# Performance work log

Measured on AMD Instinct MI355X. Metric: run time of the kernel, lower is better.

## Reference

```python
import jax, jax.numpy as jnp
from jax import lax
import numpy as np

DN = ('NCHW', 'OIHW', 'NCHW')
LEAKY_SLOPE = 0.01  # torch nn.LeakyReLU default


def conv(x, w, b=None, stride=1, pad=0):
    y = lax.conv_general_dilated(x, w, (stride, stride), [(pad, pad), (pad, pad)],
                                 dimension_numbers=DN)
    return y if b is None else y + b[None, :, None, None]


def conv_transpose2d(x, w, b):
    # torch ConvTranspose2d(k=4, s=2, p=1); w layout (Cin, Cout, 4, 4)
    wf = jnp.transpose(jnp.flip(w, (2, 3)), (1, 0, 2, 3))  # -> OIHW
    y = lax.conv_general_dilated(x, wf, (1, 1), [(2, 2), (2, 2)],
                                 lhs_dilation=(2, 2), dimension_numbers=DN)
    return y + b[None, :, None, None]


def residual_stack(x, rw3, rw1):
    # 6 ResidualLayers: x + conv1x1(relu(conv3x3(x))), both convs bias-free
    for i in range(rw3.shape[0]):
        h = jax.nn.relu(conv(x, rw3[i], pad=1))
        x = x + conv(h, rw1[i])
    return x


def vector_quantize(latents, codebook):
    # latents: [B, D, H, W] -> NHWC
    lat = jnp.transpose(latents, (0, 2, 3, 1))
    B, H, W, D = lat.shape
    flat = lat.reshape(-1, D)  # [N, D]
    # pairwise squared distances [N, K]
    dist = (jnp.sum(flat ** 2, axis=1, keepdims=True)
            + jnp.sum(codebook ** 2, axis=1)
            - 2.0 * flat @ codebook.T)
    inds = jnp.argmin(dist, axis=1)            # [N]
    q = codebook[inds].reshape(B, H, W, D)     # gather == one-hot matmul
    commitment_loss = jnp.mean((lax.stop_gradient(q) - lat) ** 2)
    embedding_loss = jnp.mean((q - lax.stop_gradient(lat)) ** 2)
    q_st = lat + lax.stop_gradient(q - lat)    # straight-through
    return jnp.transpose(q_st, (0, 3, 1, 2)), embedding_loss, commitment_loss


def setup_inputs() -> dict:
    key = jax.random.key(0)
    ks = iter(jax.random.split(key, 32))
    B, C, S = 16, 3, 128
    H0, H1 = 128, 256          # hidden_dims
    D, K = 64, 512             # embedding_dim, num_embeddings
    n_res = 6

    def w(shape, scale=0.05):
        return (jax.random.normal(next(ks), shape, dtype=jnp.float32) * scale)

    inp = {
        'x': jax.random.normal(next(ks), (B, C, S, S), dtype=jnp.float32),
        # encoder
        'ew0': w((H0, C, 4, 4)), 'eb0': jnp.zeros((H0,), jnp.float32),
        'ew1': w((H1, H0, 4, 4)), 'eb1': jnp.zeros((H1,), jnp.float32),
        'ew2': w((H1, H1, 3, 3)), 'eb2': jnp.zeros((H1,), jnp.float32),
        'erw3': w((n_res, H1, H1, 3, 3)),
        'erw1': w((n_res, H1, H1, 1, 1)),
        'ew3': w((D, H1, 1, 1)), 'eb3': jnp.zeros((D,), jnp.float32),
        # codebook, uniform(-1/K, 1/K) as in torch init
        'codebook': jax.random.uniform(next(ks), (K, D), jnp.float32, -1.0 / K, 1.0 / K),
        # decoder
        'dw0': w((H1, D, 3, 3)), 'db0': jnp.zeros((H1,), jnp.float32),
        'drw3': w((n_res, H1, H1, 3, 3)),
        'drw1': w((n_res, H1, H1, 1, 1)),
        'tw0': w((H1, H0, 4, 4)), 'tb0': jnp.zeros((H0,), jnp.float32),
        'tw1': w((H0, C, 4, 4)), 'tb1': jnp.zeros((C,), jnp.float32),
    }
    return inp


def reference(x, ew0, eb0, ew1, eb1, ew2, eb2, erw3, erw1, ew3, eb3,
              codebook, dw0, db0, drw3, drw1, tw0, tb0, tw1, tb1):
    lrelu = lambda t: jax.nn.leaky_relu(t, LEAKY_SLOPE)
    # encoder: two stride-2 downsamples, conv3x3, 6 residuals, 1x1 -> D
    h = lrelu(conv(x, ew0, eb0, stride=2, pad=1))   # [B,128,64,64]
    h = lrelu(conv(h, ew1, eb1, stride=2, pad=1))   # [B,256,32,32]
    h = lrelu(conv(h, ew2, eb2, stride=1, pad=1))
    h = residual_stack(h, erw3, erw1)
    h = lrelu(h)
    z = lrelu(conv(h, ew3, eb3))                    # [B,64,32,32]
    # vector quantization
    q, embedding_loss, commitment_loss = vector_quantize(z, codebook)
    # decoder
    d = lrelu(conv(q, dw0, db0, stride=1, pad=1))   # [B,256,32,32]
    d = residual_stack(d, drw3, drw1)
    d = lrelu(d)
    d = lrelu(conv_transpose2d(d, tw0, tb0))        # [B,128,64,64]
    recons = jnp.tanh(conv_transpose2d(d, tw1, tb1))  # [B,3,128,128]
    return recons, embedding_loss, commitment_loss
```

## Files before the change

### kernel.cpp

```cpp
#include <hip/hip_runtime.h>
#include <math.h>


typedef __attribute__((ext_vector_type(8))) short bf16x8;
typedef __attribute__((ext_vector_type(4))) float f32x4;

__device__ __forceinline__ float bf2f(short s) {
    unsigned u = ((unsigned)(unsigned short)s) << 16;
    return __builtin_bit_cast(float, u);
}
__device__ __forceinline__ unsigned short f2bfu(float f) {
    unsigned u = __builtin_bit_cast(unsigned, f);
    u = (u + 0x7fff + ((u >> 16) & 1)) >> 16;
    return (unsigned short)u;
}
__device__ __forceinline__ short f2bf(float f) { return (short)f2bfu(f); }
__device__ __forceinline__ int pack2(float a, float b) {
    return (int)f2bfu(a) | ((int)f2bfu(b) << 16);
}

template<int ACT>
__device__ __forceinline__ float actf(float v) {
    if (ACT == 1) return fmaxf(v, 0.f);
    if (ACT == 2) return v > 0.f ? v : 0.01f * v;
    return v;
}

__device__ __forceinline__ void gload_lds16(const void* g, void* l) {
    __builtin_amdgcn_global_load_lds(
        (const __attribute__((address_space(1))) unsigned int*)g,
        (__attribute__((address_space(3))) unsigned int*)l, 16, 0, 0);
}

__device__ __forceinline__ int fof(int r) { return (r & 3) ^ ((r >> 2) & 3); }

#define WAITV(N) asm volatile("s_waitcnt vmcnt(" #N ")" ::: "memory")
#define LGKM0 asm volatile("s_waitcnt lgkmcnt(0)" ::: "memory")

__device__ __forceinline__ void prep_t(const float* __restrict__ src,
        short* __restrict__ dst, int COUT, int CIN, int T, int TP,
        int blk, float* sT, int tid) {
    int opc = COUT >> 2;
    int c = blk / opc, oc0 = (blk - c * opc) * 4;
    const float* s = src + ((size_t)c * COUT + oc0) * CIN * T;
    int n = 4 * CIN * T;
    for (int i = tid; i < n; i += 256) {
        int ocl = i / (CIN * T); int rem = i - ocl * (CIN * T);
        int ic = rem / T, t = rem - ic * T;
        sT[(ocl * CIN + ic) * TP + t] = s[i];
    }
    __syncthreads();
    for (int i = tid; i < n; i += 256) {
        int t = i / (4 * CIN); int rem = i - t * (4 * CIN);
        int ocl = rem / CIN, ic = rem - ocl * CIN;
        dst[(((size_t)c * T + t) * COUT + oc0 + ocl) * CIN + ic]
            = f2bf(sT[(ocl * CIN + ic) * TP + t]);
    }
    __syncthreads();
}

__global__ __launch_bounds__(256) void prep_all_k(
        const float* ew1, const float* ew2, const float* erw3,
        const float* erw1, const float* ew3, const float* dw0,
        const float* drw3, const float* drw1, const float* tw0,
        short* Wp1, short* We2, short* Wer3, short* We11, short* Wz,
        short* Wd0, short* Wdr3, short* Wdr1, short* Wt0) {
    __shared__ float sT[9216];
    int bid = blockIdx.x, tid = threadIdx.x;
    if (bid < 64)        prep_t(ew1, Wp1, 256, 128, 16, 17, bid, sT, tid);
    else if (bid < 128)  prep_t(ew2, We2, 256, 256, 9, 9, bid - 64, sT, tid);
    else if (bid < 512)  prep_t(erw3, Wer3, 256, 256, 9, 9, bid - 128, sT, tid);
    else if (bid < 896)  prep_t(erw1, We11, 256, 256, 1, 1, bid - 512, sT, tid);
    else if (bid < 912)  prep_t(ew3, Wz, 64, 256, 1, 1, bid - 896, sT, tid);
    else if (bid < 976)  prep_t(dw0, Wd0, 256, 64, 9, 9, bid - 912, sT, tid);
    else if (bid < 1360) prep_t(drw3, Wdr3, 256, 256, 9, 9, bid - 976, sT, tid);
    else if (bid < 1744) prep_t(drw1, Wdr1, 256, 256, 1, 1, bid - 1360, sT, tid);
    else {
        int i = (bid - 1744) * 256 + tid;
        if (i < 524288) {
            int ic = i & 255; int r = i >> 8;
            int oc = r & 127; r >>= 7;
            int tap = r & 3; int par = r >> 2;
            int py = par >> 1, px = par & 1, my = tap >> 1, mx = tap & 1;
            int ky = 2 * my + (py ^ 1), kx = 2 * mx + (px ^ 1);
            Wt0[i] = f2bf(tw0[(((size_t)ic * 128 + oc) * 4 + ky) * 4 + kx]);
        }
    }
}

__global__ __launch_bounds__(256) void halo_all_k(short* P0, short* PB,
        short* PC, short* Pq) {
    int g = blockIdx.x * 256 + threadIdx.x;
    short* base; int W, C, idx;
    if (g < 135168)      { base = P0; W = 68; C = 128; idx = g; }
    else if (g < 274432) { base = PB; W = 36; C = 256; idx = g - 135168; }
    else if (g < 413696) { base = PC; W = 36; C = 256; idx = g - 274432; }
    else                 { base = Pq; W = 36; C = 64;  idx = g - 413696; }
    int c8 = C >> 3;
    int per_img = (4 * W + (W - 4) * 4) * c8;
    int img = idx / per_img, r = idx - img * per_img;
    int row, off;
    if (r < 4 * W * c8) {
        int rr = r / (W * c8);
        row = (rr < 2) ? rr : W - 4 + rr;
        off = r - rr * (W * c8);
    } else {
        int r2 = r - 4 * W * c8;
        row = 2 + r2 / (4 * c8);
        int q = r2 - (row - 2) * (4 * c8);
        off = (q < 2 * c8) ? q : (W - 2) * c8 + (q - 2 * c8);
    }
    ((int4*)(base + ((size_t)img * W + row) * W * C))[off] = int4{0, 0, 0, 0};
}

template<int CIN, int NTAPS, int TAPPAT, int SM, int INW, int OUTACT,
         bool HASB, bool FUSE>
__global__ __launch_bounds__(1024, 1) void rconv_k(
        const short* __restrict__ in, const short* __restrict__ Wp,
        const float* __restrict__ bias, const short* __restrict__ W1p,
        short* __restrict__ outp) {
    constexpr int CH64 = (CIN >= 128) ? CIN / 64 : 1;
    constexpr int LG2 = (CH64 == 4) ? 2 : (CH64 == 2) ? 1 : 0;
    constexpr int ST = NTAPS * CH64;
    __shared__ short sLds[81920];
    const int tid = threadIdx.x;
    const int lane = tid & 63, wv = tid >> 6;
    const int wc = wv & 3, mh = (wv >> 2) & 1, kg = wv >> 3;
    const int pix0 = blockIdx.x * 64;
    const int l15 = lane & 15, hi = lane >> 4;
    const int sl = hi ^ fof(l15);
    const bool low = (tid < 512);

    const short* Aptr = in;
    if (low) {
        int arow = tid >> 3, aslot = tid & 7;
        int pixa = pix0 + arow;
        int ba = pixa >> 10, Ya = (pixa >> 5) & 31, Xa = pixa & 31;
        Aptr = in + (size_t)((ba * INW + SM * Ya + 2) * INW + (SM * Xa + 2)) * CIN
             + (aslot >> 2) * 32 + (((aslot & 3) ^ fof(arow)) * 8);
    }
    const short* Bptr[2];
#pragma unroll
    for (int j = 0; j < 2; j++) {
        int gb = tid + 1024 * j;
        int kkb = gb >> 10, oc = (gb >> 2) & 255, slb = gb & 3;
        Bptr[j] = Wp + (size_t)oc * CIN + kkb * 32 + ((slb ^ fof(oc)) * 8);
    }

    auto stage = [&](int s, int bi) {
        int t = s >> LG2;
        int c0 = (s & (CH64 - 1)) * 64;
        int rof, cof;
        if (TAPPAT == 1) { rof = t / 3 - 1; cof = t % 3 - 1; }
        else             { rof = (t >> 2) - 1; cof = (t & 3) - 1; }
        char* L = (char*)sLds + bi * 40960;
        if (low)
            gload_lds16(Aptr + (rof * INW + cof) * CIN + c0, L + tid * 16);
        int woff = t * (256 * CIN) + c0;
        gload_lds16(Bptr[0] + woff, L + 8192 + tid * 16);
        gload_lds16(Bptr[1] + woff, L + 8192 + (tid + 1024) * 16);
    };

    f32x4 acc[2][4];
#pragma unroll
    for (int mi = 0; mi < 2; mi++)
#pragma unroll
        for (int ni = 0; ni < 4; ni++) acc[mi][ni] = f32x4{0.f, 0.f, 0.f, 0.f};

    stage(0, 0);
    stage(1, 1);
    int bi = 0;
    for (int s = 0; s < ST; ++s) {
        if (s < ST - 1) { if (low) { WAITV(3); } else { WAITV(2); } }
        else { WAITV(0); }
        __builtin_amdgcn_s_barrier();
        int nx = bi + 2; if (nx >= 3) nx -= 3;
        if (s + 2 < ST) stage(s + 2, nx);
        const short* LA = sLds + bi * 20480;
        const short* LB = LA + 4096;
        bf16x8 af[2], bfr[4];
#pragma unroll
        for (int mi = 0; mi < 2; mi++)
            af[mi] = *(const bf16x8*)(LA + (mh * 32 + mi * 16 + l15) * 64
                                      + kg * 32 + sl * 8);
#pragma unroll
        for (int ni = 0; ni < 4; ni++)
            bfr[ni] = *(const bf16x8*)(LB + kg * 8192
                                       + (wc * 64 + ni * 16 + l15) * 32 + sl * 8);
        __builtin_amdgcn_s_setprio(1);
#pragma unroll
        for (int mi = 0; mi < 2; mi++)
#pragma unroll
            for (int ni = 0; ni < 4; ni++)
                acc[mi][ni] = __builtin_amdgcn_mfma_f32_16x16x32_bf16(
                    af[mi], bfr[ni], acc[mi][ni], 0, 0, 0);
        __builtin_amdgcn_s_setprio(0);
        bi = (bi == 2) ? 0 : bi + 1;
    }

    float* MB = (float*)sLds;

    __syncthreads();
    if (kg == 1) {
#pragma unroll
        for (int mi = 0; mi < 2; mi++)
#pragma unroll
            for (int ni = 0; ni < 4; ni++)
#pragma unroll
                for (int r = 0; r < 4; r++)
                    MB[(mh * 32 + mi * 16 + hi * 4 + r) * 256
                       + wc * 64 + ni * 16 + l15] = acc[mi][ni][r];
    }
    __syncthreads();

    if (!FUSE) {
        if (kg == 0) {
#pragma unroll
            for (int mi = 0; mi < 2; mi++)
#pragma unroll
                for (int ni = 0; ni < 4; ni++) {
                    int col = wc * 64 + ni * 16 + l15;
                    float b = HASB ? bias[col] : 0.f;
#pragma unroll
                    for (int r = 0; r < 4; r++) {
                        int row = mh * 32 + mi * 16 + hi * 4 + r;
                        MB[row * 256 + col] += acc[mi][ni][r] + b;
                    }
                }
        }
        __syncthreads();
#pragma unroll
        for (int j = 0; j < 2; j++) {
            int idx = j * 1024 + tid;
            int p = idx >> 5, c0 = (idx & 31) * 8;
            int pix = pix0 + p;
            int b = pix >> 10, Y = (pix >> 5) & 31, X = pix & 31;
            size_t base = (((size_t)b * 36 + Y + 2) * 36 + X + 2) * 256 + c0;
            const float4* m4 = (const float4*)(MB + p * 256 + c0);
            float4 lo = m4[0], hv = m4[1];
            int pk[4];
            pk[0] = pack2(actf<OUTACT>(lo.x), actf<OUTACT>(lo.y));
            pk[1] = pack2(actf<OUTACT>(lo.z), actf<OUTACT>(lo.w));
            pk[2] = pack2(actf<OUTACT>(hv.x), actf<OUTACT>(hv.y));
            pk[3] = pack2(actf<OUTACT>(hv.z), actf<OUTACT>(hv.w));
            *(int4*)(outp + base) = *(int4*)pk;
        }
        return;
    }

    const short* W1ptr[2];
#pragma unroll
    for (int j = 0; j < 2; j++) {
        int gb = tid + 1024 * j;
        int kkb = gb >> 10, oc = (gb >> 2) & 255, slb = gb & 3;
        W1ptr[j] = W1p + (size_t)oc * 256 + kkb * 32 + ((slb ^ fof(oc)) * 8);
    }
    auto stage2 = [&](int c) {
        char* L = (char*)sLds + 98304 + (c & 1) * 32768;
        gload_lds16(W1ptr[0] + c * 64, L + tid * 16);
        gload_lds16(W1ptr[1] + c * 64, L + (tid + 1024) * 16);
    };
    stage2(0);
    stage2(1);

    short* H = sLds + 32768;
    if (kg == 0) {
#pragma unroll
        for (int mi = 0; mi < 2; mi++)
#pragma unroll
            for (int ni = 0; ni < 4; ni++) {
                int col = wc * 64 + ni * 16 + l15;
#pragma unroll
                for (int r = 0; r < 4; r++) {
                    int row = mh * 32 + mi * 16 + hi * 4 + r;
                    float v = acc[mi][ni][r] + MB[row * 256 + col];
                    H[((col >> 5) * 64 + row) * 32
                      + (((col >> 3) & 3) ^ fof(row)) * 8 + (col & 7)]
                        = f2bf(fmaxf(v, 0.f));
                }
            }
    }
    LGKM0;
    __builtin_amdgcn_sched_barrier(0);
    __builtin_amdgcn_s_barrier();

    f32x4 acc2[2][4];
#pragma unroll
    for (int mi = 0; mi < 2; mi++)
#pragma unroll
        for (int ni = 0; ni < 4; ni++) acc2[mi][ni] = f32x4{0.f, 0.f, 0.f, 0.f};

    for (int s2 = 0; s2 < 4; ++s2) {
        if (s2 < 3) { WAITV(2); } else { WAITV(0); }
        __builtin_amdgcn_s_barrier();
        int c = s2 * 2 + kg;
        const short* LW = sLds + 49152 + (s2 & 1) * 16384 + kg * 8192;
        bf16x8 af2[2], bf2r[4];
#pragma unroll
        for (int mi = 0; mi < 2; mi++) {
            int row = mh * 32 + mi * 16 + l15;
            af2[mi] = *(const bf16x8*)(H + (c * 64 + row) * 32
                                       + (hi ^ fof(row)) * 8);
        }
#pragma unroll
        for (int ni = 0; ni < 4; ni++)
            bf2r[ni] = *(const bf16x8*)(LW + (wc * 64 + ni * 16 + l15) * 32
                                        + sl * 8);
        LGKM0;
        __builtin_amdgcn_sched_barrier(0);
        __builtin_amdgcn_s_barrier();
        if (s2 < 2) stage2(s2 + 2);
        __builtin_amdgcn_s_setprio(1);
#pragma unroll
        for (int mi = 0; mi < 2; mi++)
#pragma unroll
            for (int ni = 0; ni < 4; ni++)
                acc2[mi][ni] = __builtin_amdgcn_mfma_f32_16x16x32_bf16(
                    af2[mi], bf2r[ni], acc2[mi][ni], 0, 0, 0);
        __builtin_amdgcn_s_setprio(0);
    }

    __syncthreads();
    if (kg == 1) {
#pragma unroll
        for (int mi = 0; mi < 2; mi++)
#pragma unroll
            for (int ni = 0; ni < 4; ni++)
#pragma unroll
                for (int r = 0; r < 4; r++)
                    MB[(mh * 32 + mi * 16 + hi * 4 + r) * 256
                       + wc * 64 + ni * 16 + l15] = acc2[mi][ni][r];
    }
    __syncthreads();
    if (kg == 0) {
#pragma unroll
        for (int mi = 0; mi < 2; mi++)
#pragma unroll
            for (int ni = 0; ni < 4; ni++) {
                int col = wc * 64 + ni * 16 + l15;
#pragma unroll
                for (int r = 0; r < 4; r++) {
                    int row = mh * 32 + mi * 16 + hi * 4 + r;
                    MB[row * 256 + col] += acc2[mi][ni][r];
                }
            }
    }
    __syncthreads();
#pragma unroll
    for (int j = 0; j < 2; j++) {
        int idx = j * 1024 + tid;
        int p = idx >> 5, c0 = (idx & 31) * 8;
        int pix = pix0 + p;
        int b = pix >> 10, Y = (pix >> 5) & 31, X = pix & 31;
        size_t base = (((size_t)b * 36 + Y + 2) * 36 + X + 2) * 256 + c0;
        const float4* m4 = (const float4*)(MB + p * 256 + c0);
        float4 lo = m4[0], hv = m4[1];
        bf16x8 rv = *(const bf16x8*)(in + base);
        int pk[4];
        pk[0] = pack2(actf<OUTACT>(lo.x + bf2f(rv[0])),
                      actf<OUTACT>(lo.y + bf2f(rv[1])));
        pk[1] = pack2(actf<OUTACT>(lo.z + bf2f(rv[2])),
                      actf<OUTACT>(lo.w + bf2f(rv[3])));
        pk[2] = pack2(actf<OUTACT>(hv.x + bf2f(rv[4])),
                      actf<OUTACT>(hv.y + bf2f(rv[5])));
        pk[3] = pack2(actf<OUTACT>(hv.z + bf2f(rv[6])),
                      actf<OUTACT>(hv.w + bf2f(rv[7])));
        *(int4*)(outp + base) = *(int4*)pk;
    }
}

template<int CIN, int COUT, int NTAPS, int TAPPAT, int SM, int INW,
         int OUTACT, bool RES, bool HASB, int OUTMODE, int BN>
__global__ __launch_bounds__(256) void gconv_k(
        const short* __restrict__ in, const short* __restrict__ Wp,
        const float* __restrict__ bias, const short* __restrict__ res,
        void* __restrict__ outp) {
    constexpr int KCH = CIN / 32;
    constexpr int LG = (KCH == 8) ? 3 : (KCH == 4) ? 2 : (KCH == 2) ? 1 : 0;
    constexpr int ST = NTAPS * KCH;
    constexpr int NF = BN / 32;
    constexpr int WN = BN / 2;
    __shared__ short sA[3 * 128 * 32];
    __shared__ short sB[3 * BN * 32];
    const int tid = threadIdx.x;
    const int lane = tid & 63, wv = tid >> 6;
    const int wr = wv >> 1, wc = wv & 1;
    const int pix0 = blockIdx.x * 128;
    const int oc0 = blockIdx.y * BN;
    int py = 0, px = 0;
    if (TAPPAT == 3) {
        int par = blockIdx.z;
        py = par >> 1; px = par & 1;
        Wp += (size_t)par * NTAPS * COUT * CIN;
    }
    const int sp = tid >> 2;
    const int swz = ((tid & 3) ^ fof(sp)) * 8;
    int rbA[2];
#pragma unroll
    for (int rd = 0; rd < 2; rd++) {
        int pix = pix0 + sp + rd * 64;
        int b = pix >> 10, Y = (pix >> 5) & 31, X = pix & 31;
        rbA[rd] = ((b * INW + SM * Y + 2) * INW + (SM * X + 2)) * CIN + swz;
    }
    const int wb0 = (oc0 + sp) * CIN + swz;
    const int wb1 = (oc0 + sp + 64) * CIN + swz;

    f32x4 acc[4][NF];
#pragma unroll
    for (int i = 0; i < 4; i++)
#pragma unroll
        for (int j = 0; j < NF; j++) acc[i][j] = f32x4{0.f, 0.f, 0.f, 0.f};

    const int sslot = ((lane >> 4) ^ fof(lane & 15)) * 8;
    const int abase = (wr * 64 + (lane & 15)) * 32 + sslot;
    const int bbase = (wc * WN + (lane & 15)) * 32 + sslot;

    auto stage = [&](int s, int biq) {
        int t = s >> LG, c = s & (KCH - 1);
        int rof, cof;
        if (TAPPAT == 0) { rof = 0; cof = 0; }
        else if (TAPPAT == 1) { rof = t / 3 - 1; cof = t % 3 - 1; }
        else if (TAPPAT == 2) { rof = t / 4 - 1; cof = t % 4 - 1; }
        else { int my = t >> 1, mx = t & 1;
               rof = (py == 0) ? -my : 1 - my;
               cof = (px == 0) ? -mx : 1 - mx; }
        const int tapoff = (rof * INW + cof) * CIN + c * 32;
        char* a = (char*)sA + biq * 8192;
        char* b = (char*)sB + biq * (BN * 64);
        const short* wt = Wp + (size_t)t * COUT * CIN + c * 32;
        gload_lds16(in + rbA[0] + tapoff, a + tid * 16);
        gload_lds16(in + rbA[1] + tapoff, a + 4096 + tid * 16);
        gload_lds16(wt + wb0, b + tid * 16);
        if (BN == 128) gload_lds16(wt + wb1, b + 4096 + tid * 16);
    };

    stage(0, 0);
    stage(1, 1);
    int cur = 0;
    for (int s = 0; s < ST; ++s) {
        if (s < ST - 1) {
            if (BN == 128) { WAITV(4); } else { WAITV(3); }
        } else {
            WAITV(0);
        }
        __builtin_amdgcn_s_barrier();
        int nxt = cur + 2; if (nxt >= 3) nxt -= 3;
        if (s + 2 < ST) stage(s + 2, nxt);
        const short* a = sA + cur * 4096;
        const short* b = sB + cur * (BN * 32);
        bf16x8 af[4], bfm[NF];
#pragma unroll
        for (int mi = 0; mi < 4; mi++)
            af[mi] = *(const bf16x8*)(a + abase + mi * 512);
#pragma unroll
        for (int ni = 0; ni < NF; ni++)
            bfm[ni] = *(const bf16x8*)(b + bbase + ni * 512);
        __builtin_amdgcn_s_setprio(1);
#pragma unroll
        for (int mi = 0; mi < 4; mi++)
#pragma unroll
            for (int ni = 0; ni < NF; ni++)
                acc[mi][ni] = __builtin_amdgcn_mfma_f32_16x16x32_bf16(
                    af[mi], bfm[ni], acc[mi][ni], 0, 0, 0);
        __builtin_amdgcn_s_setprio(0);
        cur = (cur == 2) ? 0 : cur + 1;
    }
#pragma unroll
    for (int mi = 0; mi < 4; mi++) {
#pragma unroll
        for (int r = 0; r < 4; r++) {
            int pix = pix0 + wr * 64 + mi * 16 + (lane >> 4) * 4 + r;
            int b = pix >> 10, Y = (pix >> 5) & 31, X = pix & 31;
            size_t rowoff = 0;
            if (OUTMODE == 0)
                rowoff = (((size_t)b * 36 + Y + 2) * 36 + X + 2) * COUT;
            else if (OUTMODE == 2)
                rowoff = (((size_t)b * 68 + 2 * Y + py + 2) * 68 + 2 * X + px + 2) * 128;
#pragma unroll
            for (int ni = 0; ni < NF; ni++) {
                int col = oc0 + wc * WN + ni * 16 + (lane & 15);
                float v = acc[mi][ni][r];
                if (HASB) v += bias[col];
                if (OUTMODE == 1) {
                    ((float*)outp)[(size_t)pix * COUT + col] = actf<OUTACT>(v);
                } else {
                    size_t off = rowoff + col;
                    if (RES) v += bf2f(res[off]);
                    ((short*)outp)[off] = f2bf(actf<OUTACT>(v));
                }
            }
        }
    }
}

__global__ __launch_bounds__(256) void conv0_k(const float* __restrict__ x,
        const float* __restrict__ W, const float* __restrict__ bias,
        short* __restrict__ P0) {
    __shared__ float sP[3 * 4 * 132];
    __shared__ short sB[8192];
    __shared__ float sMB[8192];
    int y = blockIdx.x, b = blockIdx.y;
    int tid = threadIdx.x;
    int lane = tid & 63, w = tid >> 6;
    int l15 = lane & 15, hi = lane >> 4;
    int sl = hi ^ fof(l15);
    for (int t = tid; t < 8192; t += 256) {
        int oc = t >> 6, k = t & 63;
        float v = (k < 48) ? W[(size_t)oc * 48 + k] : 0.f;
        int kk = k >> 5, slot = (k >> 3) & 3, j = k & 7;
        sB[oc * 64 + kk * 32 + ((slot ^ fof(oc)) * 8) + j] = f2bf(v);
    }
    for (int t = tid; t < 1560; t += 256) {
        int ic = t / 520; int r = t - ic * 520;
        int ry = r / 130, rx = r - ry * 130;
        int iy = 2 * y - 1 + ry, ix = rx - 1;
        float v = 0.f;
        if ((unsigned)iy < 128u && (unsigned)ix < 128u)
            v = x[((size_t)b * 3 + ic) * 16384 + iy * 128 + ix];
        sP[(ic * 4 + ry) * 132 + rx] = v;
    }
    __syncthreads();
    int ox = w * 16 + l15;
    bf16x8 af[2];
#pragma unroll
    for (int kk = 0; kk < 2; kk++) {
        short tmp[8];
#pragma unroll
        for (int j = 0; j < 8; j++) {
            int k = kk * 32 + hi * 8 + j;
            float v = 0.f;
            if (k < 48) {
                int ic = k >> 4, ky = (k >> 2) & 3, kx = k & 3;
                v = sP[(ic * 4 + ky) * 132 + 2 * ox + kx];
            }
            tmp[j] = f2bf(v);
        }
        af[kk] = *(bf16x8*)tmp;
    }
    f32x4 acc[8];
#pragma unroll
    for (int ni = 0; ni < 8; ni++) acc[ni] = f32x4{0.f, 0.f, 0.f, 0.f};
#pragma unroll
    for (int ni = 0; ni < 8; ni++) {
        int oc = ni * 16 + l15;
        bf16x8 b0 = *(const bf16x8*)(sB + oc * 64 + sl * 8);
        bf16x8 b1 = *(const bf16x8*)(sB + oc * 64 + 32 + sl * 8);
        acc[ni] = __builtin_amdgcn_mfma_f32_16x16x32_bf16(af[0], b0, acc[ni], 0, 0, 0);
        acc[ni] = __builtin_amdgcn_mfma_f32_16x16x32_bf16(af[1], b1, acc[ni], 0, 0, 0);
    }
#pragma unroll
    for (int ni = 0; ni < 8; ni++) {
        int col = ni * 16 + l15;
        float bv = bias[col];
#pragma unroll
        for (int r = 0; r < 4; r++)
            sMB[(w * 16 + hi * 4 + r) * 128 + col] = actf<2>(acc[ni][r] + bv);
    }
    __syncthreads();
#pragma unroll
    for (int it = 0; it < 4; it++) {
        int idx = it * 256 + tid;
        int p = idx >> 4, c0 = (idx & 15) * 8;
        size_t base = (((size_t)b * 68 + y + 2) * 68 + p + 2) * 128 + c0;
        const float4* m4 = (const float4*)(sMB + p * 128 + c0);
        float4 lo = m4[0], hv = m4[1];
        int pk[4];
        pk[0] = pack2(lo.x, lo.y); pk[1] = pack2(lo.z, lo.w);
        pk[2] = pack2(hv.x, hv.y); pk[3] = pack2(hv.z, hv.w);
        *(int4*)(P0 + base) = *(int4*)pk;
    }
}

__global__ __launch_bounds__(256) void vq_argmin_k(const float* __restrict__ zr,
        const float* __restrict__ cb, int* __restrict__ ind) {
    __shared__ short sZ[2][128 * 32];
    __shared__ short sC[2][128 * 32];
    __shared__ float sN[128];
    const int tid = threadIdx.x;
    const int lane = tid & 63, wv = tid >> 6;
    const int pos0 = blockIdx.x * 128;
#pragma unroll
    for (int it = 0; it < 4; ++it) {
        int task = tid + it * 256;
        int row = task >> 3, kq = task & 7;
        const float4* zp = (const float4*)(zr + (size_t)(pos0 + row) * 64 + kq * 8);
        float4 v0 = zp[0], v1 = zp[1];
        int slot = ((kq & 3) ^ fof(row)) * 8;
        short tmp[8] = {f2bf(v0.x), f2bf(v0.y), f2bf(v0.z), f2bf(v0.w),
                        f2bf(v1.x), f2bf(v1.y), f2bf(v1.z), f2bf(v1.w)};
        *(bf16x8*)&sZ[kq >> 2][row * 32 + slot] = *(bf16x8*)tmp;
    }
    const int sslot = ((lane >> 4) ^ fof(lane & 15)) * 8;
    const int l15 = lane & 15;
    float best[2][4]; int bidx[2][4];
#pragma unroll
    for (int mi = 0; mi < 2; mi++)
#pragma unroll
        for (int r = 0; r < 4; r++) { best[mi][r] = INFINITY; bidx[mi][r] = 0; }
    for (int ch = 0; ch < 4; ++ch) {
        __syncthreads();
#pragma unroll
        for (int it = 0; it < 4; ++it) {
            int task = tid + it * 256;
            int row = task >> 3, kq = task & 7;
            const float4* cp = (const float4*)(cb + (size_t)(ch * 128 + row) * 64 + kq * 8);
            float4 v0 = cp[0], v1 = cp[1];
            int slot = ((kq & 3) ^ fof(row)) * 8;
            short tmp[8] = {f2bf(v0.x), f2bf(v0.y), f2bf(v0.z), f2bf(v0.w),
                            f2bf(v1.x), f2bf(v1.y), f2bf(v1.z), f2bf(v1.w)};
            *(bf16x8*)&sC[kq >> 2][row * 32 + slot] = *(bf16x8*)tmp;
        }
        if (tid < 128) {
            const float4* cp = (const float4*)(cb + (size_t)(ch * 128 + tid) * 64);
            float s = 0.f;
#pragma unroll
            for (int q = 0; q < 16; q++) {
                float4 v = cp[q];
                s += v.x * v.x + v.y * v.y + v.z * v.z + v.w * v.w;
            }
            sN[tid] = s;
        }
        __syncthreads();
        f32x4 acc[2][8];
#pragma unroll
        for (int mi = 0; mi < 2; mi++)
#pragma unroll
            for (int ni = 0; ni < 8; ni++) acc[mi][ni] = f32x4{0.f, 0.f, 0.f, 0.f};
#pragma unroll
        for (int kc = 0; kc < 2; ++kc) {
            bf16x8 za[2], ca[8];
#pragma unroll
            for (int mi = 0; mi < 2; mi++)
                za[mi] = *(const bf16x8*)&sZ[kc][(wv * 32 + mi * 16 + l15) * 32 + sslot];
#pragma unroll
            for (int ni = 0; ni < 8; ni++)
                ca[ni] = *(const bf16x8*)&sC[kc][(ni * 16 + l15) * 32 + sslot];
#pragma unroll
            for (int mi = 0; mi < 2; mi++)
#pragma unroll
                for (int ni = 0; ni < 8; ni++)
                    acc[mi][ni] = __builtin_amdgcn_mfma_f32_16x16x32_bf16(
                        za[mi], ca[ni], acc[mi][ni], 0, 0, 0);
        }
#pragma unroll
        for (int mi = 0; mi < 2; mi++)
#pragma unroll
            for (int ni = 0; ni < 8; ni++) {
                float nrm = sN[ni * 16 + l15];
                int idx = ch * 128 + ni * 16 + l15;
#pragma unroll
                for (int r = 0; r < 4; r++) {
                    float sc = nrm - 2.f * acc[mi][ni][r];
                    if (sc < best[mi][r]) { best[mi][r] = sc; bidx[mi][r] = idx; }
                }
            }
    }
#pragma unroll
    for (int m = 1; m < 16; m <<= 1) {
#pragma unroll
        for (int mi = 0; mi < 2; mi++)
#pragma unroll
            for (int r = 0; r < 4; r++) {
                float os = __shfl_xor(best[mi][r], m);
                int   oi = __shfl_xor(bidx[mi][r], m);
                if (os < best[mi][r] || (os == best[mi][r] && oi < bidx[mi][r])) {
                    best[mi][r] = os; bidx[mi][r] = oi;
                }
            }
    }
    if (l15 == 0) {
        int g = lane >> 4;
#pragma unroll
        for (int mi = 0; mi < 2; mi++)
#pragma unroll
            for (int r = 0; r < 4; r++)
                ind[pos0 + wv * 32 + mi * 16 + g * 4 + r] = bidx[mi][r];
    }
}

__global__ __launch_bounds__(256) void vq_gather_k(const float* __restrict__ zr,
        const float* __restrict__ cb, const int* __restrict__ ind,
        short* __restrict__ q, float* __restrict__ part) {
    int pos = blockIdx.x * 256 + threadIdx.x;
    int b = pos >> 10, hw = pos & 1023, y = hw >> 5, xx = hw & 31;
    int idx = ind[pos];
    const float4* cp = (const float4*)(cb + (size_t)idx * 64);
    const float4* zp = (const float4*)(zr + (size_t)pos * 64);
    size_t qb = (((size_t)b * 36 + y + 2) * 36 + xx + 2) * 64;
    float sum = 0.f;
#pragma unroll
    for (int d4 = 0; d4 < 16; d4++) {
        float4 c = cp[d4], z = zp[d4];
        float dx = c.x - z.x, dy = c.y - z.y, dz = c.z - z.z, dw = c.w - z.w;
        sum += dx * dx + dy * dy + dz * dz + dw * dw;
        ((int*)(q + qb))[2 * d4] = pack2(c.x, c.y);
        ((int*)(q + qb))[2 * d4 + 1] = pack2(c.z, c.w);
    }
#pragma unroll
    for (int m = 1; m < 64; m <<= 1) sum += __shfl_xor(sum, m);
    __shared__ float sred[4];
    int lane = threadIdx.x & 63, wvv = threadIdx.x >> 6;
    if (lane == 0) sred[wvv] = sum;
    __syncthreads();
    if (threadIdx.x == 0)
        part[blockIdx.x] = sred[0] + sred[1] + sred[2] + sred[3];
}

__global__ void finalize_k(const float* __restrict__ part, float* __restrict__ out) {
    if (threadIdx.x == 0) {
        float s = 0.f;
        for (int k = 0; k < 64; k++) s += part[k];
        float m = s / 1048576.f;
        out[786432] = m;
        out[786433] = m;
    }
}

__global__ __launch_bounds__(256) void tw1_k(const short* __restrict__ in,
        const float* __restrict__ W, const float* __restrict__ bias,
        float* __restrict__ out) {
    __shared__ float sW[16 * 128 * 4];
    int b = blockIdx.y, y0 = blockIdx.x * 8;
    int tid = threadIdx.x;
    for (int t = tid; t < 2048; t += 256) {
        int k = t >> 7, ic = t & 127;
        float4 v;
        v.x = W[((size_t)ic * 3 + 0) * 16 + k];
        v.y = W[((size_t)ic * 3 + 1) * 16 + k];
        v.z = W[((size_t)ic * 3 + 2) * 16 + k];
        v.w = 0.f;
        *(float4*)&sW[t * 4] = v;
    }
    __syncthreads();
    int r = tid >> 5, g = tid & 31;
    int oy = y0 + r, py = oy & 1, Y = oy >> 1, pxp = g & 1;
    float acc[4][3];
#pragma unroll
    for (int p = 0; p < 4; p++)
#pragma unroll
        for (int o = 0; o < 3; o++) acc[p][o] = 0.f;
#pragma unroll
    for (int my = 0; my < 2; my++) {
        int iy = Y + ((py == 0) ? -my : 1 - my) + 2;
        const short* rowp = in + (((size_t)b * 68 + iy) * 68) * 128;
        int ky = 2 * my + (py ^ 1);
#pragma unroll
        for (int mx = 0; mx < 2; mx++) {
            int kx = 2 * mx + (pxp ^ 1);
            int cof = ((pxp == 0) ? -mx : 1 - mx) + 2;
            const float* wbase = &sW[((ky * 4 + kx) * 128) * 4];
            const short* pptr[4];
#pragma unroll
            for (int p = 0; p < 4; p++) {
                int X = ((g + 32 * p) >> 1) + cof;
                pptr[p] = rowp + (size_t)X * 128;
            }
            for (int icb = 0; icb < 16; icb++) {
                bf16x8 v[4];
#pragma unroll
                for (int p = 0; p < 4; p++)
                    v[p] = *(const bf16x8*)(pptr[p] + icb * 8);
#pragma unroll
                for (int j = 0; j < 8; j++) {
                    float4 w = *(const float4*)&wbase[(icb * 8 + j) * 4];
#pragma unroll
                    for (int p = 0; p < 4; p++) {
                        float xv = bf2f(v[p][j]);
                        acc[p][0] += w.x * xv;
                        acc[p][1] += w.y * xv;
                        acc[p][2] += w.z * xv;
                    }
                }
            }
        }
    }
#pragma unroll
    for (int p = 0; p < 4; p++) {
        int ox = g + 32 * p;
#pragma unroll
        for (int o = 0; o < 3; o++)
            out[(((size_t)b * 3 + o) << 14) + oy * 128 + ox] =
                tanhf(acc[p][o] + bias[o]);
    }
}

extern "C" void kernel_launch(void* const* d_in, const int* in_sizes, int n_in,
                              void* d_out, int out_size, void* d_ws, size_t ws_size,
                              hipStream_t stream) {
    const float* x    = (const float*)d_in[0];
    const float* ew0  = (const float*)d_in[1];
    const float* eb0  = (const float*)d_in[2];
    const float* ew1  = (const float*)d_in[3];
    const float* eb1  = (const float*)d_in[4];
    const float* ew2  = (const float*)d_in[5];
    const float* eb2  = (const float*)d_in[6];
    const float* erw3 = (const float*)d_in[7];
    const float* erw1 = (const float*)d_in[8];
    const float* ew3  = (const float*)d_in[9];
    const float* eb3  = (const float*)d_in[10];
    const float* cbk  = (const float*)d_in[11];
    const float* dw0  = (const float*)d_in[12];
    const float* db0  = (const float*)d_in[13];
    const float* drw3 = (const float*)d_in[14];
    const float* drw1 = (const float*)d_in[15];
    const float* tw0  = (const float*)d_in[16];
    const float* tb0  = (const float*)d_in[17];
    const float* tw1  = (const float*)d_in[18];
    const float* tb1  = (const float*)d_in[19];
    float* out = (float*)d_out;

    short* S = (short*)d_ws;
    short* P0  = S;
    short* PB  = P0 + 9469952;
    short* PC  = PB + 5308416;
    short* Pq  = PC + 5308416;
    short* Wp1 = Pq + 1327104;
    short* We2 = Wp1 + 524288;
    short* Wer3 = We2 + 589824;
    short* We11 = Wer3 + 3538944;
    short* Wz   = We11 + 393216;
    short* Wd0  = Wz + 16384;
    short* Wdr3 = Wd0 + 147456;
    short* Wdr1 = Wdr3 + 3538944;
    short* Wt0  = Wdr1 + 393216;
    float* F   = (float*)(S + 31080448);
    float* Zr  = F;
    float* PART = Zr + 1048576;
    int*   IND = (int*)(PART + 64);

    halo_all_k<<<1752, 256, 0, stream>>>(P0, PB, PC, Pq);
    prep_all_k<<<3792, 256, 0, stream>>>(ew1, ew2, erw3, erw1, ew3, dw0,
        drw3, drw1, tw0, Wp1, We2, Wer3, We11, Wz, Wd0, Wdr3, Wdr1, Wt0);

    conv0_k<<<dim3(64, 16), 256, 0, stream>>>(x, ew0, eb0, P0);
    rconv_k<128, 16, 2, 2, 68, 2, true, false>
        <<<256, 1024, 0, stream>>>(P0, Wp1, eb1, nullptr, PB);
    rconv_k<256, 9, 1, 1, 36, 2, true, false>
        <<<256, 1024, 0, stream>>>(PB, We2, eb2, nullptr, PC);
    for (int i = 0; i < 6; i++) {
        short* inb  = (i & 1) ? PB : PC;
        short* outb = (i & 1) ? PC : PB;
        if (i < 5)
            rconv_k<256, 9, 1, 1, 36, 0, false, true>
                <<<256, 1024, 0, stream>>>(inb, Wer3 + (size_t)i * 589824,
                    nullptr, We11 + (size_t)i * 65536, outb);
        else
            rconv_k<256, 9, 1, 1, 36, 2, false, true>
                <<<256, 1024, 0, stream>>>(inb, Wer3 + (size_t)i * 589824,
                    nullptr, We11 + (size_t)i * 65536, outb);
    }
    gconv_k<256, 64, 1, 0, 1, 36, 2, false, true, 1, 64>
        <<<dim3(128, 1), 256, 0, stream>>>(PC, Wz, eb3, nullptr, Zr);

    vq_argmin_k<<<128, 256, 0, stream>>>(Zr, cbk, IND);
    vq_gather_k<<<64, 256, 0, stream>>>(Zr, cbk, IND, Pq, PART);

    rconv_k<64, 9, 1, 1, 36, 2, true, false>
        <<<256, 1024, 0, stream>>>(Pq, Wd0, db0, nullptr, PC);
    for (int i = 0; i < 6; i++) {
        short* inb  = (i & 1) ? PB : PC;
        short* outb = (i & 1) ? PC : PB;
        if (i < 5)
            rconv_k<256, 9, 1, 1, 36, 0, false, true>
                <<<256, 1024, 0, stream>>>(inb, Wdr3 + (size_t)i * 589824,
                    nullptr, Wdr1 + (size_t)i * 65536, outb);
        else
            rconv_k<256, 9, 1, 1, 36, 2, false, true>
                <<<256, 1024, 0, stream>>>(inb, Wdr3 + (size_t)i * 589824,
                    nullptr, Wdr1 + (size_t)i * 65536, outb);
    }
    gconv_k<256, 128, 4, 3, 1, 36, 2, false, true, 2, 128>
        <<<dim3(128, 1, 4), 256, 0, stream>>>(PC, Wt0, tb0, nullptr, P0);
    tw1_k<<<dim3(16, 16), 256, 0, stream>>>(P0, tw1, tb1, out);

    finalize_k<<<1, 64, 0, stream>>>(PART, out);
}
```

Measured before the change: 591.5 us.

## Drop split-K wave groups in rconv_k, use 512-thread blocks with double buffering

The residual/conv kernel drops the two-way K split across wave groups in 1024-thread blocks. It now uses 512-thread blocks where each wave runs the full K loop, two 64-wide k-steps per stage. This removes the LDS partial-sum reduction and its extra barriers in both the 3x3 and fused 1x1 phases, and halves LDS use. In exchange there are half as many waves per CU on a 256-block grid. The load pipeline also goes from triple to double buffering with a full wait each step, and the tighter launch bound may raise register pressure.

```diff
diff --git a/kernel.cpp b/kernel.cpp
--- a/kernel.cpp
+++ b/kernel.cpp
@@ -115,34 +115,33 @@
 
 template<int CIN, int NTAPS, int TAPPAT, int SM, int INW, int OUTACT,
          bool HASB, bool FUSE>
-__global__ __launch_bounds__(1024, 1) void rconv_k(
+__global__ __launch_bounds__(512, 4) void rconv_k(
         const short* __restrict__ in, const short* __restrict__ Wp,
         const float* __restrict__ bias, const short* __restrict__ W1p,
         short* __restrict__ outp) {
     constexpr int CH64 = (CIN >= 128) ? CIN / 64 : 1;
     constexpr int LG2 = (CH64 == 4) ? 2 : (CH64 == 2) ? 1 : 0;
     constexpr int ST = NTAPS * CH64;
-    __shared__ short sLds[81920];
+    __shared__ short sLds[40960];
     const int tid = threadIdx.x;
     const int lane = tid & 63, wv = tid >> 6;
-    const int wc = wv & 3, mh = (wv >> 2) & 1, kg = wv >> 3;
+    const int wc = wv & 3, mh = wv >> 2;
     const int pix0 = blockIdx.x * 64;
     const int l15 = lane & 15, hi = lane >> 4;
     const int sl = hi ^ fof(l15);
-    const bool low = (tid < 512);
-
-    const short* Aptr = in;
-    if (low) {
-        int arow = tid >> 3, aslot = tid & 7;
+
+    const int arow = tid >> 3, aslot = tid & 7;
+    const short* Aptr;
+    {
         int pixa = pix0 + arow;
         int ba = pixa >> 10, Ya = (pixa >> 5) & 31, Xa = pixa & 31;
         Aptr = in + (size_t)((ba * INW + SM * Ya + 2) * INW + (SM * Xa + 2)) * CIN
              + (aslot >> 2) * 32 + (((aslot & 3) ^ fof(arow)) * 8);
     }
-    const short* Bptr[2];
-#pragma unroll
-    for (int j = 0; j < 2; j++) {
-        int gb = tid + 1024 * j;
+    const short* Bptr[4];
+#pragma unroll
+    for (int j = 0; j < 4; j++) {
+        int gb = tid + 512 * j;
         int kkb = gb >> 10, oc = (gb >> 2) & 255, slb = gb & 3;
         Bptr[j] = Wp + (size_t)oc * CIN + kkb * 32 + ((slb ^ fof(oc)) * 8);
     }
@@ -154,11 +153,11 @@
         if (TAPPAT == 1) { rof = t / 3 - 1; cof = t % 3 - 1; }
         else             { rof = (t >> 2) - 1; cof = (t & 3) - 1; }
         char* L = (char*)sLds + bi * 40960;
-        if (low)
-            gload_lds16(Aptr + (rof * INW + cof) * CIN + c0, L + tid * 16);
+        gload_lds16(Aptr + (rof * INW + cof) * CIN + c0, L + tid * 16);
         int woff = t * (256 * CIN) + c0;
-        gload_lds16(Bptr[0] + woff, L + 8192 + tid * 16);
-        gload_lds16(Bptr[1] + woff, L + 8192 + (tid + 1024) * 16);
+#pragma unroll
+        for (int j = 0; j < 4; j++)
+            gload_lds16(Bptr[j] + woff, L + 8192 + (tid + 512 * j) * 16);
     };
 
     f32x4 acc[2][4];
@@ -168,70 +167,53 @@
         for (int ni = 0; ni < 4; ni++) acc[mi][ni] = f32x4{0.f, 0.f, 0.f, 0.f};
 
     stage(0, 0);
-    stage(1, 1);
-    int bi = 0;
     for (int s = 0; s < ST; ++s) {
-        if (s < ST - 1) { if (low) { WAITV(3); } else { WAITV(2); } }
-        else { WAITV(0); }
+        WAITV(0);
         __builtin_amdgcn_s_barrier();
-        int nx = bi + 2; if (nx >= 3) nx -= 3;
-        if (s + 2 < ST) stage(s + 2, nx);
-        const short* LA = sLds + bi * 20480;
-        const short* LB = LA + 4096;
-        bf16x8 af[2], bfr[4];
+        if (s + 1 < ST) stage(s + 1, (s + 1) & 1);
+        const char* L = (const char*)sLds + (s & 1) * 40960;
+        bf16x8 af[2][2], bfr[4][2];
+#pragma unroll
+        for (int kk = 0; kk < 2; kk++) {
+#pragma unroll
+            for (int mi = 0; mi < 2; mi++)
+                af[mi][kk] = *(const bf16x8*)(L
+                    + (mh * 32 + mi * 16 + l15) * 128 + kk * 64 + sl * 16);
+#pragma unroll
+            for (int ni = 0; ni < 4; ni++)
+                bfr[ni][kk] = *(const bf16x8*)(L + 8192 + kk * 16384
+                    + (wc * 64 + ni * 16 + l15) * 64 + sl * 16);
+        }
+        __builtin_amdgcn_s_setprio(1);
+#pragma unroll
+        for (int kk = 0; kk < 2; kk++)
+#pragma unroll
+            for (int mi = 0; mi < 2; mi++)
+#pragma unroll
+                for (int ni = 0; ni < 4; ni++)
+                    acc[mi][ni] = __builtin_amdgcn_mfma_f32_16x16x32_bf16(
+                        af[mi][kk], bfr[ni][kk], acc[mi][ni], 0, 0, 0);
+        __builtin_amdgcn_s_setprio(0);
+    }
+
+    if (!FUSE) {
+        __syncthreads();
+        float* MB = (float*)sLds;
 #pragma unroll
         for (int mi = 0; mi < 2; mi++)
-            af[mi] = *(const bf16x8*)(LA + (mh * 32 + mi * 16 + l15) * 64
-                                      + kg * 32 + sl * 8);
-#pragma unroll
-        for (int ni = 0; ni < 4; ni++)
-            bfr[ni] = *(const bf16x8*)(LB + kg * 8192
-                                       + (wc * 64 + ni * 16 + l15) * 32 + sl * 8);
-        __builtin_amdgcn_s_setprio(1);
-#pragma unroll
-        for (int mi = 0; mi < 2; mi++)
-#pragma unroll
-            for (int ni = 0; ni < 4; ni++)
-                acc[mi][ni] = __builtin_amdgcn_mfma_f32_16x16x32_bf16(
-                    af[mi], bfr[ni], acc[mi][ni], 0, 0, 0);
-        __builtin_amdgcn_s_setprio(0);
-        bi = (bi == 2) ? 0 : bi + 1;
-    }
-
-    float* MB = (float*)sLds;
-
-    __syncthreads();
-    if (kg == 1) {
-#pragma unroll
-        for (int mi = 0; mi < 2; mi++)
-#pragma unroll
-            for (int ni = 0; ni < 4; ni++)
+#pragma unroll
+            for (int ni = 0; ni < 4; ni++) {
+                int col = wc * 64 + ni * 16 + l15;
+                float b = HASB ? bias[col] : 0.f;
 #pragma unroll
                 for (int r = 0; r < 4; r++)
-                    MB[(mh * 32 + mi * 16 + hi * 4 + r) * 256
-                       + wc * 64 + ni * 16 + l15] = acc[mi][ni][r];
-    }
-    __syncthreads();
-
-    if (!FUSE) {
-        if (kg == 0) {
-#pragma unroll
-            for (int mi = 0; mi < 2; mi++)
-#pragma unroll
-                for (int ni = 0; ni < 4; ni++) {
-                    int col = wc * 64 + ni * 16 + l15;
-                    float b = HASB ? bias[col] : 0.f;
-#pragma unroll
-                    for (int r = 0; r < 4; r++) {
-                        int row = mh * 32 + mi * 16 + hi * 4 + r;
-                        MB[row * 256 + col] += acc[mi][ni][r] + b;
-                    }
-                }
-        }
+                    MB[(mh * 32 + mi * 16 + hi * 4 + r) * 256 + col]
+                        = acc[mi][ni][r] + b;
+            }
         __syncthreads();
 #pragma unroll
-        for (int j = 0; j < 2; j++) {
-            int idx = j * 1024 + tid;
+        for (int j = 0; j < 4; j++) {
+            int idx = j * 512 + tid;
             int p = idx >> 5, c0 = (idx & 31) * 8;
             int pix = pix0 + p;
             int b = pix >> 10, Y = (pix >> 5) & 31, X = pix & 31;
@@ -248,68 +230,63 @@
         return;
     }
 
+    short* H = sLds;
+    __syncthreads();
+#pragma unroll
+    for (int mi = 0; mi < 2; mi++)
+#pragma unroll
+        for (int ni = 0; ni < 4; ni++) {
+            int col = wc * 64 + ni * 16 + l15;
+#pragma unroll
+            for (int r = 0; r < 4; r++) {
+                int row = mh * 32 + mi * 16 + hi * 4 + r;
+                H[((col >> 5) * 64 + row) * 32
+                  + (((col >> 3) & 3) ^ fof(row)) * 8 + (col & 7)]
+                    = f2bf(fmaxf(acc[mi][ni][r], 0.f));
+            }
+        }
     const short* W1ptr[2];
 #pragma unroll
     for (int j = 0; j < 2; j++) {
-        int gb = tid + 1024 * j;
-        int kkb = gb >> 10, oc = (gb >> 2) & 255, slb = gb & 3;
-        W1ptr[j] = W1p + (size_t)oc * 256 + kkb * 32 + ((slb ^ fof(oc)) * 8);
+        int gb = tid + 512 * j;
+        int oc = gb >> 2, slb = gb & 3;
+        W1ptr[j] = W1p + (size_t)oc * 256 + ((slb ^ fof(oc)) * 8);
     }
     auto stage2 = [&](int c) {
-        char* L = (char*)sLds + 98304 + (c & 1) * 32768;
-        gload_lds16(W1ptr[0] + c * 64, L + tid * 16);
-        gload_lds16(W1ptr[1] + c * 64, L + (tid + 1024) * 16);
+        char* L = (char*)sLds + 32768 + (c & 1) * 16384;
+        gload_lds16(W1ptr[0] + c * 32, L + tid * 16);
+        gload_lds16(W1ptr[1] + c * 32, L + (tid + 512) * 16);
     };
+    LGKM0;
+    __builtin_amdgcn_sched_barrier(0);
+    __syncthreads();
     stage2(0);
     stage2(1);
 
-    short* H = sLds + 32768;
-    if (kg == 0) {
-#pragma unroll
-        for (int mi = 0; mi < 2; mi++)
-#pragma unroll
-            for (int ni = 0; ni < 4; ni++) {
-                int col = wc * 64 + ni * 16 + l15;
-#pragma unroll
-                for (int r = 0; r < 4; r++) {
-                    int row = mh * 32 + mi * 16 + hi * 4 + r;
-                    float v = acc[mi][ni][r] + MB[row * 256 + col];
-                    H[((col >> 5) * 64 + row) * 32
-                      + (((col >> 3) & 3) ^ fof(row)) * 8 + (col & 7)]
-                        = f2bf(fmaxf(v, 0.f));
-                }
-            }
-    }
-    LGKM0;
-    __builtin_amdgcn_sched_barrier(0);
-    __builtin_amdgcn_s_barrier();
-
     f32x4 acc2[2][4];
 #pragma unroll
     for (int mi = 0; mi < 2; mi++)
 #pragma unroll
         for (int ni = 0; ni < 4; ni++) acc2[mi][ni] = f32x4{0.f, 0.f, 0.f, 0.f};
 
-    for (int s2 = 0; s2 < 4; ++s2) {
-        if (s2 < 3) { WAITV(2); } else { WAITV(0); }
+    for (int c = 0; c < 8; ++c) {
+        if (c < 7) { WAITV(2); } else { WAITV(0); }
         __builtin_amdgcn_s_barrier();
-        int c = s2 * 2 + kg;
-        const short* LW = sLds + 49152 + (s2 & 1) * 16384 + kg * 8192;
+        const char* LW = (const char*)sLds + 32768 + (c & 1) * 16384;
         bf16x8 af2[2], bf2r[4];
 #pragma unroll
         for (int mi = 0; mi < 2; mi++) {
             int row = mh * 32 + mi * 16 + l15;
-            af2[mi] = *(const bf16x8*)(H + (c * 64 + row) * 32
-                                       + (hi ^ fof(row)) * 8);
+            af2[mi] = *(const bf16x8*)&H[(c * 64 + row) * 32 + sl * 8];
         }
 #pragma unroll
         for (int ni = 0; ni < 4; ni++)
-            bf2r[ni] = *(const bf16x8*)(LW + (wc * 64 + ni * 16 + l15) * 32
-                                        + sl * 8);
+            bf2r[ni] = *(const bf16x8*)(LW
+                + (wc * 64 + ni * 16 + l15) * 64 + sl * 16);
         LGKM0;
         __builtin_amdgcn_sched_barrier(0);
         __builtin_amdgcn_s_barrier();
-        if (s2 < 2) stage2(s2 + 2);
+        if (c < 6) stage2(c + 2);
         __builtin_amdgcn_s_setprio(1);
 #pragma unroll
         for (int mi = 0; mi < 2; mi++)
@@ -321,34 +298,21 @@
     }
 
     __syncthreads();
-    if (kg == 1) {
-#pragma unroll
-        for (int mi = 0; mi < 2; mi++)
-#pragma unroll
-            for (int ni = 0; ni < 4; ni++)
-#pragma unroll
-                for (int r = 0; r < 4; r++)
-                    MB[(mh * 32 + mi * 16 + hi * 4 + r) * 256
-                       + wc * 64 + ni * 16 + l15] = acc2[mi][ni][r];
-    }
-    __syncthreads();
-    if (kg == 0) {
-#pragma unroll
-        for (int mi = 0; mi < 2; mi++)
-#pragma unroll
-            for (int ni = 0; ni < 4; ni++) {
-                int col = wc * 64 + ni * 16 + l15;
-#pragma unroll
-                for (int r = 0; r < 4; r++) {
-                    int row = mh * 32 + mi * 16 + hi * 4 + r;
-                    MB[row * 256 + col] += acc2[mi][ni][r];
-                }
-            }
-    }
-    __syncthreads();
-#pragma unroll
-    for (int j = 0; j < 2; j++) {
-        int idx = j * 1024 + tid;
+    float* MB = (float*)sLds;
+#pragma unroll
+    for (int mi = 0; mi < 2; mi++)
+#pragma unroll
+        for (int ni = 0; ni < 4; ni++) {
+            int col = wc * 64 + ni * 16 + l15;
+#pragma unroll
+            for (int r = 0; r < 4; r++)
+                MB[(mh * 32 + mi * 16 + hi * 4 + r) * 256 + col]
+                    = acc2[mi][ni][r];
+        }
+    __syncthreads();
+#pragma unroll
+    for (int j = 0; j < 4; j++) {
+        int idx = j * 512 + tid;
         int p = idx >> 5, c0 = (idx & 31) * 8;
         int pix = pix0 + p;
         int b = pix >> 10, Y = (pix >> 5) & 31, X = pix & 31;
@@ -834,19 +798,19 @@
 
     conv0_k<<<dim3(64, 16), 256, 0, stream>>>(x, ew0, eb0, P0);
     rconv_k<128, 16, 2, 2, 68, 2, true, false>
-        <<<256, 1024, 0, stream>>>(P0, Wp1, eb1, nullptr, PB);
+        <<<256, 512, 0, stream>>>(P0, Wp1, eb1, nullptr, PB);
     rconv_k<256, 9, 1, 1, 36, 2, true, false>
-        <<<256, 1024, 0, stream>>>(PB, We2, eb2, nullptr, PC);
+        <<<256, 512, 0, stream>>>(PB, We2, eb2, nullptr, PC);
     for (int i = 0; i < 6; i++) {
         short* inb  = (i & 1) ? PB : PC;
         short* outb = (i & 1) ? PC : PB;
         if (i < 5)
             rconv_k<256, 9, 1, 1, 36, 0, false, true>
-                <<<256, 1024, 0, stream>>>(inb, Wer3 + (size_t)i * 589824,
+                <<<256, 512, 0, stream>>>(inb, Wer3 + (size_t)i * 589824,
                     nullptr, We11 + (size_t)i * 65536, outb);
         else
             rconv_k<256, 9, 1, 1, 36, 2, false, true>
-                <<<256, 1024, 0, stream>>>(inb, Wer3 + (size_t)i * 589824,
+                <<<256, 512, 0, stream>>>(inb, Wer3 + (size_t)i * 589824,
                     nullptr, We11 + (size_t)i * 65536, outb);
     }
     gconv_k<256, 64, 1, 0, 1, 36, 2, false, true, 1, 64>
@@ -856,17 +820,17 @@
     vq_gather_k<<<64, 256, 0, stream>>>(Zr, cbk, IND, Pq, PART);
 
     rconv_k<64, 9, 1, 1, 36, 2, true, false>
-        <<<256, 1024, 0, stream>>>(Pq, Wd0, db0, nullptr, PC);
+        <<<256, 512, 0, stream>>>(Pq, Wd0, db0, nullptr, PC);
     for (int i = 0; i < 6; i++) {
         short* inb  = (i & 1) ? PB : PC;
         short* outb = (i & 1) ? PC : PB;
         if (i < 5)
             rconv_k<256, 9, 1, 1, 36, 0, false, true>
-                <<<256, 1024, 0, stream>>>(inb, Wdr3 + (size_t)i * 589824,
+                <<<256, 512, 0, stream>>>(inb, Wdr3 + (size_t)i * 589824,
                     nullptr, Wdr1 + (size_t)i * 65536, outb);
         else
             rconv_k<256, 9, 1, 1, 36, 2, false, true>
-                <<<256, 1024, 0, stream>>>(inb, Wdr3 + (size_t)i * 589824,
+                <<<256, 512, 0, stream>>>(inb, Wdr3 + (size_t)i * 589824,
                     nullptr, Wdr1 + (size_t)i * 65536, outb);
     }
     gconv_k<256, 128, 4, 3, 1, 36, 2, false, true, 2, 128>
```

Result: no change. 596.4 us (+0.8%).
